# Kernel optimization log

Hardware: AMD Instinct MI355X
Metric: run time of the kernel (lower is better)

Reference implementation:

```python
import jax, jax.numpy as jnp
import numpy as np

BSZ = 2          # batch
H_IMG = 180      # BEV height
W_IMG = 180      # BEV width
BLK = 15         # block_size
D = 128          # d_model
NH = 8           # nhead
DH = D // NH     # head dim


def _bn_relu(x, g, b, m, v, eps=1e-5):
    # eval-mode BatchNorm2d followed by ReLU; x is NCHW
    s = g * jax.lax.rsqrt(v + eps)
    return jax.nn.relu((x - m[None, :, None, None]) * s[None, :, None, None]
                       + b[None, :, None, None])


def _split_tokens(x):
    # (B,C,H,W) -> (B*nb, blk*blk, C), block order = (row-block, col-block)
    B, C, H, W = x.shape
    hb, wb = H // BLK, W // BLK
    x = x.reshape(B, C, hb, BLK, wb, BLK)
    x = x.transpose(0, 2, 4, 1, 3, 5)              # (B,hb,wb,C,blk,blk)
    x = x.reshape(B * hb * wb, C, BLK * BLK)
    return x.transpose(0, 2, 1)                    # (B*nb, L, C)


def _merge_tokens(t, B, H, W):
    # (B*nb, L, C) -> (B,C,H,W), inverse of _split_tokens
    hb, wb = H // BLK, W // BLK
    C = t.shape[-1]
    x = t.transpose(0, 2, 1).reshape(B, hb, wb, C, BLK, BLK)
    x = x.transpose(0, 3, 1, 4, 2, 5)              # (B,C,hb,blk,wb,blk)
    return x.reshape(B, C, H, W)


def setup_inputs() -> dict:
    key = jax.random.key(0)
    ks = jax.random.split(key, 16)
    n = lambda i, shp, sc=0.05: jax.random.normal(ks[i], shp, jnp.float32) * sc
    inp = {
        'camera_feat': jax.random.normal(ks[0], (BSZ, 80, H_IMG, W_IMG), jnp.float32),
        'lidar_feat': jax.random.normal(ks[1], (BSZ, 256, H_IMG, W_IMG), jnp.float32),
        'cam_w': n(2, (D, 80)),
        'cam_gamma': jnp.ones((D,), jnp.float32),
        'cam_beta': jnp.zeros((D,), jnp.float32),
        'cam_mean': n(3, (D,)),
        'cam_var': jax.random.uniform(ks[4], (D,), jnp.float32, 0.5, 1.5),
        'lidar_w': n(5, (D, 256)),
        'lidar_gamma': jnp.ones((D,), jnp.float32),
        'lidar_beta': jnp.zeros((D,), jnp.float32),
        'lidar_mean': n(6, (D,)),
        'lidar_var': jax.random.uniform(ks[7], (D,), jnp.float32, 0.5, 1.5),
        'in_proj_w': n(8, (3 * D, D)),
        'in_proj_b': jnp.zeros((3 * D,), jnp.float32),
        'out_proj_w': n(9, (D, D)),
        'out_proj_b': jnp.zeros((D,), jnp.float32),
        'outc_w': n(10, (256, D, 3, 3)),
        'outc_gamma': jnp.ones((256,), jnp.float32),
        'outc_beta': jnp.zeros((256,), jnp.float32),
        'outc_mean': n(11, (256,)),
        'outc_var': jax.random.uniform(ks[12], (256,), jnp.float32, 0.5, 1.5),
    }
    return inp


def reference(camera_feat, lidar_feat,
              cam_w, cam_gamma, cam_beta, cam_mean, cam_var,
              lidar_w, lidar_gamma, lidar_beta, lidar_mean, lidar_var,
              in_proj_w, in_proj_b, out_proj_w, out_proj_b,
              outc_w, outc_gamma, outc_beta, outc_mean, outc_var):
    B, _, H, W = camera_feat.shape
    # 1x1 conv projections + BN + ReLU
    cam_p = _bn_relu(jnp.einsum('bchw,dc->bdhw', camera_feat, cam_w),
                     cam_gamma, cam_beta, cam_mean, cam_var)
    lid_p = _bn_relu(jnp.einsum('bchw,dc->bdhw', lidar_feat, lidar_w),
                     lidar_gamma, lidar_beta, lidar_mean, lidar_var)
    # windowed tokens: (B*nb, L=225, D)
    cam_t = _split_tokens(cam_p)
    lid_t = _split_tokens(lid_p)
    # cross-attention: query=lidar, key/value=camera (torch MHA math)
    wq, wk, wv = in_proj_w[:D], in_proj_w[D:2 * D], in_proj_w[2 * D:]
    bq, bk, bv = in_proj_b[:D], in_proj_b[D:2 * D], in_proj_b[2 * D:]
    BN, L, _ = lid_t.shape
    q = (lid_t @ wq.T + bq).reshape(BN, L, NH, DH).transpose(0, 2, 1, 3)
    k = (cam_t @ wk.T + bk).reshape(BN, L, NH, DH).transpose(0, 2, 1, 3)
    v = (cam_t @ wv.T + bv).reshape(BN, L, NH, DH).transpose(0, 2, 1, 3)
    scores = jnp.einsum('bhqd,bhkd->bhqk', q, k) / jnp.sqrt(jnp.float32(DH))
    attn = jax.nn.softmax(scores, axis=-1)
    ctx = jnp.einsum('bhqk,bhkd->bhqd', attn, v)
    ctx = ctx.transpose(0, 2, 1, 3).reshape(BN, L, D)
    attn_out = ctx @ out_proj_w.T + out_proj_b
    # merge windows back and fuse
    fused = _merge_tokens(attn_out, B, H, W) + lid_p
    # 3x3 conv + BN + ReLU
    y = jax.lax.conv_general_dilated(
        fused, outc_w, window_strides=(1, 1), padding='SAME',
        dimension_numbers=('NCHW', 'OIHW', 'NCHW'))
    return _bn_relu(y, outc_gamma, outc_beta, outc_mean, outc_var)
```

## Files before the change

kernel.cpp:

```cpp
#include <hip/hip_runtime.h>
#include <hip/hip_bf16.h>
#include <cmath>

#define HW      32400
#define WIMG    180
#define DD      128
#define NHEADS  8
#define DHEAD   16
#define LTOK    225
#define PSTRIDE 64928
#define FBROW   188
#define FBH     182
#define FBSZ    ((size_t)FBH * FBROW * 128)
#define QSCALE  0.36067376022224085f

typedef __attribute__((ext_vector_type(8))) short bf16x8;
typedef __attribute__((ext_vector_type(4))) float f32x4;

union U16B { uint4 u; int4 i; bf16x8 v; };

__device__ __forceinline__ bf16x8 ldfrag(const __hip_bfloat16* p, int ld, int lane) {
  return *(const bf16x8*)(p + (size_t)(lane & 15) * ld + ((lane >> 4) << 3));
}

__device__ __forceinline__ float bf2f(unsigned int u) {
  return __uint_as_float(u << 16);
}

__device__ __forceinline__ unsigned short f2bf(float x) {
  unsigned int b = __float_as_uint(x);
  return (unsigned short)((b + 0x7fffu + ((b >> 16) & 1u)) >> 16);
}

__global__ void k_cast(const float* __restrict__ in, __hip_bfloat16* __restrict__ out, int n) {
  int i = blockIdx.x * 256 + threadIdx.x;
  if (i < n) out[i] = __float2bfloat16(in[i]);
}

__global__ void k_prepproj(const float* __restrict__ w, __hip_bfloat16* __restrict__ wb,
                           int C, int Kpad) {
  int i = blockIdx.x * 256 + threadIdx.x;
  if (i >= 128 * Kpad) return;
  int d = i / Kpad, c = i % Kpad;
  wb[i] = (c < C) ? __float2bfloat16(w[d * C + c]) : __float2bfloat16(0.f);
}

__global__ void k_prepw2(const float* __restrict__ cw, __hip_bfloat16* __restrict__ wcb) {
  int i = blockIdx.x * 256 + threadIdx.x;
  if (i >= 294912) return;
  int oc16  = i / 18432;
  int r0    = i % 18432;
  int tap   = r0 / 2048;
  int r1    = r0 % 2048;
  int chunk = r1 / 512;
  int r2    = r1 % 512;
  int lane  = r2 / 8;
  int e     = r2 % 8;
  int oc = oc16 * 16 + (lane & 15);
  int ic = chunk * 32 + (lane >> 4) * 8 + e;
  wcb[i] = __float2bfloat16(cw[(size_t)(oc * 128 + ic) * 9 + tap]);
}

__global__ void k_zero_border(__hip_bfloat16* __restrict__ fbb) {
  int idx = blockIdx.x * 256 + threadIdx.x;
  if (idx >= 2 * 736 * 16) return;
  int b = idx / (736 * 16);
  int r = idx % (736 * 16);
  int px = r >> 4, blk = r & 15;
  int row, col;
  if (px < 188)      { row = 0;            col = px; }
  else if (px < 376) { row = 181;          col = px - 188; }
  else if (px < 556) { row = px - 376 + 1; col = 0; }
  else               { row = px - 556 + 1; col = 181; }
  ((uint4*)(fbb + (size_t)b * FBSZ + ((size_t)row * FBROW + col) * 128))[blk] =
      make_uint4(0u, 0u, 0u, 0u);
}

__global__ void __launch_bounds__(256) k_proj_mfma(
    const float* __restrict__ in, const __hip_bfloat16* __restrict__ wb,
    const float* __restrict__ g, const float* __restrict__ be,
    const float* __restrict__ mu, const float* __restrict__ var,
    __hip_bfloat16* __restrict__ outp, int C, int Kpad) {
  __shared__ __align__(16) __hip_bfloat16 sa[128 * 64];
  int m0 = blockIdx.x * 128;
  int b = blockIdx.z;
  int tid = threadIdx.x, lane = tid & 63, wid = tid >> 6;
  int wm = (wid >> 1) * 64, wn = (wid & 1) * 64;
  const float* inb = in + (size_t)b * C * HW;
  int sp = (tid >> 1) & 127;
  int sc4 = (tid & 1) * 4;
  int gp = m0 + sp;
  bool pok = gp < HW;
  f32x4 acc[4][4] = {};
  for (int kc = 0; kc < Kpad; kc += 64) {
    __syncthreads();
#pragma unroll
    for (int it = 0; it < 8; ++it) {
      int lc = sc4 + it * 8;
      int c = kc + lc;
      unsigned short u[4];
#pragma unroll
      for (int j = 0; j < 4; ++j) {
        float x = (pok && (c + j) < C) ? inb[(size_t)(c + j) * HW + gp] : 0.f;
        u[j] = f2bf(x);
      }
      int blk = (lc >> 3) ^ (sp & 7);
      char* dst = (char*)sa + sp * 128 + blk * 16 + (lc & 7) * 2;
      *(uint2*)dst = make_uint2(((unsigned)u[1] << 16) | u[0],
                                ((unsigned)u[3] << 16) | u[2]);
    }
    __syncthreads();
#pragma unroll
    for (int ks = 0; ks < 2; ++ks) {
      bf16x8 af[4], bfr[4];
#pragma unroll
      for (int i = 0; i < 4; ++i) {
        int pr = wm + i * 16 + (lane & 15);
        int blk = ((ks * 4 + (lane >> 4)) ^ (pr & 7));
        af[i] = *(const bf16x8*)((const char*)sa + pr * 128 + blk * 16);
      }
#pragma unroll
      for (int j = 0; j < 4; ++j)
        bfr[j] = ldfrag(wb + (size_t)(wn + j * 16) * Kpad + kc + ks * 32, Kpad, lane);
#pragma unroll
      for (int i = 0; i < 4; ++i)
#pragma unroll
        for (int j = 0; j < 4; ++j)
          acc[i][j] = __builtin_amdgcn_mfma_f32_16x16x32_bf16(af[i], bfr[j], acc[i][j], 0, 0, 0);
    }
  }
  int col = lane & 15, rq = lane >> 4;
  __hip_bfloat16* ob = outp + (size_t)b * PSTRIDE * 128;
#pragma unroll
  for (int j = 0; j < 4; ++j) {
    int d = wn + j * 16 + col;
    float s = g[d] * rsqrtf(var[d] + 1e-5f);
    float mm = mu[d], bb = be[d];
#pragma unroll
    for (int i = 0; i < 4; ++i) {
#pragma unroll
      for (int r = 0; r < 4; ++r) {
        int m = m0 + wm + i * 16 + rq * 4 + r;
        if (m < HW) {
          float y = (acc[i][j][r] - mm) * s + bb;
          ob[(size_t)m * 128 + d] = __float2bfloat16(fmaxf(y, 0.f));
        }
      }
    }
  }
}

__global__ void __launch_bounds__(256) k_gemm_bias(
    const __hip_bfloat16* __restrict__ A, const __hip_bfloat16* __restrict__ B,
    const float* __restrict__ bias, __hip_bfloat16* __restrict__ out,
    int K, int ldout, float oscale) {
  int m0 = blockIdx.x * 128, n0 = blockIdx.y * 128, b = blockIdx.z;
  int lane = threadIdx.x & 63, wid = threadIdx.x >> 6;
  int wm = (wid >> 1) * 64, wn = (wid & 1) * 64;
  const __hip_bfloat16* Ab = A + (size_t)b * PSTRIDE * K;
  f32x4 acc[4][4] = {};
  for (int kc = 0; kc < K; kc += 32) {
    bf16x8 af[4], bfr[4];
#pragma unroll
    for (int i = 0; i < 4; ++i)
      af[i] = ldfrag(Ab + (size_t)(m0 + wm + i * 16) * K + kc, K, lane);
#pragma unroll
    for (int j = 0; j < 4; ++j)
      bfr[j] = ldfrag(B + (size_t)(n0 + wn + j * 16) * K + kc, K, lane);
#pragma unroll
    for (int i = 0; i < 4; ++i)
#pragma unroll
      for (int j = 0; j < 4; ++j)
        acc[i][j] = __builtin_amdgcn_mfma_f32_16x16x32_bf16(af[i], bfr[j], acc[i][j], 0, 0, 0);
  }
  int col = lane & 15, rq = lane >> 4;
  __hip_bfloat16* ob = out + (size_t)b * PSTRIDE * ldout;
#pragma unroll
  for (int j = 0; j < 4; ++j) {
    int n = n0 + wn + j * 16 + col;
    float bs = bias[n];
#pragma unroll
    for (int i = 0; i < 4; ++i) {
#pragma unroll
      for (int r = 0; r < 4; ++r) {
        int m = m0 + wm + i * 16 + rq * 4 + r;
        if (m < HW) ob[(size_t)m * ldout + n] = __float2bfloat16((acc[i][j][r] + bs) * oscale);
      }
    }
  }
}

__global__ void __launch_bounds__(256) k_attn_mfma(
    const __hip_bfloat16* __restrict__ qc, const __hip_bfloat16* __restrict__ kvb,
    __hip_bfloat16* __restrict__ ctx) {
  __shared__ __align__(16) uint4 Kf[15 * 64];
  __shared__ __align__(16) uint4 Vf[15 * 64];
  __shared__ __align__(16) unsigned short psh[4 * 384];
  int bn = blockIdx.x, hh = blockIdx.y;
  int b = bn / 144, rr = bn % 144, tby = rr / 12, tbx = rr % 12;
  int tid = threadIdx.x;
  int pbase = tby * 15 * WIMG + tbx * 15;
  const __hip_bfloat16* kvbase = kvb + (size_t)b * PSTRIDE * 256 + hh * 16;

  if (tid < 240) {
    int row = tid;
    int ck = row >> 4, q = row & 15;
    uint4 k0 = make_uint4(0, 0, 0, 0), k1 = k0, v0 = k0, v1 = k0;
    if (row < LTOK) {
      int p = pbase + (row / 15) * WIMG + (row % 15);
      const uint4* kp = (const uint4*)(kvbase + (size_t)p * 256);
      k0 = kp[0]; k1 = kp[1];
      v0 = kp[16]; v1 = kp[17];
    }
    uint4 zz = make_uint4(0, 0, 0, 0);
    Kf[ck * 64 + q]      = k0;
    Kf[ck * 64 + 16 + q] = k1;
    Kf[ck * 64 + 32 + q] = zz;
    Kf[ck * 64 + 48 + q] = zz;
    unsigned short vv[16];
    *(uint4*)&vv[0] = v0;
    *(uint4*)&vv[8] = v1;
    int vg = q >> 3, vj = q & 7;
#pragma unroll
    for (int d0 = 0; d0 < 16; ++d0) {
      int d = (d0 + q + 2 * ck) & 15;
      ((unsigned short*)&Vf[ck * 64 + vg * 16 + d])[vj] = vv[d];
    }
    Vf[ck * 64 + 32 + q] = zz;
    Vf[ck * 64 + 48 + q] = zz;
  }
  __syncthreads();

  int lane = tid & 63, wid = tid >> 6;
  int g = lane >> 4, q15 = lane & 15;
  int wq0 = wid * 64;
  char* pw_base = (char*)psh + wid * 768;
  const bf16x8* KfB = (const bf16x8*)Kf + lane;
  const bf16x8* VfB = (const bf16x8*)Vf + lane;

  bf16x8 qf[4];
#pragma unroll
  for (int i = 0; i < 4; ++i) {
    int q = wq0 + i * 16 + q15;
    int qq = q < LTOK ? q : 0;
    int p = pbase + (qq / 15) * WIMG + (qq % 15);
    U16B u; u.u = make_uint4(0, 0, 0, 0);
    if (g < 2) u.u = *(const uint4*)(qc + ((size_t)b * PSTRIDE + p) * 128 + hh * 16 + g * 8);
    qf[i] = u.v;
  }

  const f32x4 zacc = {};
  float ls[4] = {0.f, 0.f, 0.f, 0.f};
  f32x4 oac[4] = {};
#pragma unroll 1
  for (int ck = 0; ck < 15; ++ck) {
    bf16x8 kf = KfB[ck * 64];
    bf16x8 vf = VfB[ck * 64];
#pragma unroll
    for (int i = 0; i < 4; ++i) {
      f32x4 st = __builtin_amdgcn_mfma_f32_16x16x32_bf16(kf, qf[i], zacc, 0, 0, 0);
      float p0 = exp2f(st[0]);
      float p1 = exp2f(st[1]);
      float p2 = exp2f(st[2]);
      float p3 = exp2f(st[3]);
      if (ck == 14) {
        if (g) p0 = 0.f;
        p1 = 0.f; p2 = 0.f; p3 = 0.f;
      }
      ls[i] += (p0 + p1) + (p2 + p3);
      unsigned w0 = (unsigned)__bfloat16_as_ushort(__float2bfloat16(p0)) |
                    ((unsigned)__bfloat16_as_ushort(__float2bfloat16(p1)) << 16);
      unsigned w1 = (unsigned)__bfloat16_as_ushort(__float2bfloat16(p2)) |
                    ((unsigned)__bfloat16_as_ushort(__float2bfloat16(p3)) << 16);
      *(uint2*)(pw_base + q15 * 48 + g * 8) = make_uint2(w0, w1);
      U16B pu;
      pu.u = *(const uint4*)(pw_base + q15 * 48 + (g & 1) * 16);
      oac[i] = __builtin_amdgcn_mfma_f32_16x16x32_bf16(vf, pu.v, oac[i], 0, 0, 0);
    }
  }
#pragma unroll
  for (int i = 0; i < 4; ++i) {
    ls[i] += __shfl_xor(ls[i], 16);
    ls[i] += __shfl_xor(ls[i], 32);
  }

  __hip_bfloat16* cb = ctx + (size_t)b * PSTRIDE * 128 + hh * 16;
#pragma unroll
  for (int i = 0; i < 4; ++i) {
    float inv = 1.f / ls[i];
    int qo = wq0 + i * 16 + q15;
    if (qo < LTOK) {
      unsigned lo = (unsigned)f2bf(oac[i][0] * inv) | ((unsigned)f2bf(oac[i][1] * inv) << 16);
      unsigned hi = (unsigned)f2bf(oac[i][2] * inv) | ((unsigned)f2bf(oac[i][3] * inv) << 16);
      int p = pbase + (qo / 15) * WIMG + (qo % 15);
      *(uint2*)(cb + (size_t)p * 128 + g * 4) = make_uint2(lo, hi);
    }
  }
}

__global__ void __launch_bounds__(256) k_outproj_mfma(
    const __hip_bfloat16* __restrict__ ctx, const __hip_bfloat16* __restrict__ wob,
    const float* __restrict__ opb, const __hip_bfloat16* __restrict__ lidb,
    __hip_bfloat16* __restrict__ fb) {
  int m0 = blockIdx.x * 128, b = blockIdx.z;
  int lane = threadIdx.x & 63, wid = threadIdx.x >> 6;
  int wm = (wid >> 1) * 64, wn = (wid & 1) * 64;
  const __hip_bfloat16* Ab = ctx + (size_t)b * PSTRIDE * 128;
  f32x4 acc[4][4] = {};
  for (int kc = 0; kc < 128; kc += 32) {
    bf16x8 af[4], bfr[4];
#pragma unroll
    for (int i = 0; i < 4; ++i)
      af[i] = ldfrag(Ab + (size_t)(m0 + wm + i * 16) * 128 + kc, 128, lane);
#pragma unroll
    for (int j = 0; j < 4; ++j)
      bfr[j] = ldfrag(wob + (size_t)(wn + j * 16) * 128 + kc, 128, lane);
#pragma unroll
    for (int i = 0; i < 4; ++i)
#pragma unroll
      for (int j = 0; j < 4; ++j)
        acc[i][j] = __builtin_amdgcn_mfma_f32_16x16x32_bf16(af[i], bfr[j], acc[i][j], 0, 0, 0);
  }
  int col = lane & 15, rq = lane >> 4;
  const __hip_bfloat16* lb = lidb + (size_t)b * PSTRIDE * 128;
  __hip_bfloat16* fbp = fb + (size_t)b * FBSZ;
#pragma unroll
  for (int j = 0; j < 4; ++j) {
    int n = wn + j * 16 + col;
    float bs = opb[n];
#pragma unroll
    for (int i = 0; i < 4; ++i) {
#pragma unroll
      for (int r = 0; r < 4; ++r) {
        int m = m0 + wm + i * 16 + rq * 4 + r;
        if (m < HW) {
          float v = acc[i][j][r] + bs + __bfloat162float(lb[(size_t)m * 128 + n]);
          int hhh = m / WIMG, www = m % WIMG;
          fbp[((size_t)(hhh + 1) * FBROW + (www + 1)) * 128 + n] = __float2bfloat16(v);
        }
      }
    }
  }
}

__global__ void __launch_bounds__(512) k_conv_mfma(
    const __hip_bfloat16* __restrict__ fb, const __hip_bfloat16* __restrict__ wcb,
    const float* __restrict__ g, const float* __restrict__ be,
    const float* __restrict__ mu, const float* __restrict__ var,
    float* __restrict__ out) {
  __shared__ __align__(16) uint4 Asm[4 * 16 * 62];
  int bx = blockIdx.x;
  int hp = bx / 3, strip = bx % 3;
  int h0 = hp * 2;
  int w0 = strip * 60;
  int b = blockIdx.z;
  int tid = threadIdx.x, lane = tid & 63, wid = tid >> 6;
  int q15 = lane & 15, kg = lane >> 4;
  int wpx = (wid & 1) * 32;
  int ocq = wid >> 1;
  const __hip_bfloat16* fbb = fb + (size_t)b * FBSZ;
  const __hip_bfloat16* Bw = wcb + (size_t)(ocq * 4) * 18432 + lane * 8;

#pragma unroll
  for (int it = 0; it < 8; ++it) {
    int slot = it * 512 + tid;
    if (slot < 3968) {
      int px = slot % 62;
      int rowk = slot / 62;
      int dy = rowk >> 4, kgrp = rowk & 15;
      Asm[slot] = *(const uint4*)(fbb + ((size_t)(h0 + dy) * FBROW + (w0 + px)) * 128 + kgrp * 8);
    }
  }

#define LOADB(dst, t)                                                          \
  {                                                                            \
    int tap_ = (t) >> 2, ch_ = (t) & 3;                                        \
    _Pragma("unroll") for (int j = 0; j < 4; ++j)                              \
        dst[j] = *(const bf16x8*)(Bw + (size_t)j * 18432 + tap_ * 2048 + ch_ * 512); \
  }

  bf16x8 bp0[4], bp1[4];
  LOADB(bp0, 0);
  LOADB(bp1, 1);
  __syncthreads();

  f32x4 acc[2][2][4] = {};

#define STEP(t, bp)                                                            \
  {                                                                            \
    int tap_ = (t) >> 2, ch_ = (t) & 3;                                        \
    int dy_ = tap_ / 3, dx_ = tap_ % 3;                                        \
    bf16x8 af[2][2];                                                           \
    _Pragma("unroll") for (int r = 0; r < 2; ++r) {                            \
      int rowk_ = ((dy_ + r) * 16 + ch_ * 4 + kg) * 62;                        \
      _Pragma("unroll") for (int i = 0; i < 2; ++i)                            \
          af[r][i] = *(const bf16x8*)&Asm[rowk_ + wpx + i * 16 + q15 + dx_];   \
    }                                                                          \
    _Pragma("unroll") for (int r = 0; r < 2; ++r)                              \
        _Pragma("unroll") for (int i = 0; i < 2; ++i)                          \
            _Pragma("unroll") for (int j = 0; j < 4; ++j)                      \
                acc[r][i][j] = __builtin_amdgcn_mfma_f32_16x16x32_bf16(af[r][i], bp[j], acc[r][i][j], 0, 0, 0); \
  }

#pragma unroll
  for (int t = 0; t < 36; t += 2) {
    STEP(t, bp0);
    if (t + 2 < 36) LOADB(bp0, t + 2);
    STEP(t + 1, bp1);
    if (t + 3 < 36) LOADB(bp1, t + 3);
  }
#undef STEP
#undef LOADB

  int ocbase = ocq * 64;
#pragma unroll
  for (int j = 0; j < 4; ++j) {
    int oc = ocbase + j * 16 + q15;
    float s = g[oc] * rsqrtf(var[oc] + 1e-5f);
    float mm = mu[oc], bb = be[oc];
#pragma unroll
    for (int r = 0; r < 2; ++r) {
#pragma unroll
      for (int i = 0; i < 2; ++i) {
        int pxb = wpx + i * 16 + kg * 4;
        if (pxb < 60) {
          float4 o4;
          o4.x = fmaxf((acc[r][i][j][0] - mm) * s + bb, 0.f);
          o4.y = fmaxf((acc[r][i][j][1] - mm) * s + bb, 0.f);
          o4.z = fmaxf((acc[r][i][j][2] - mm) * s + bb, 0.f);
          o4.w = fmaxf((acc[r][i][j][3] - mm) * s + bb, 0.f);
          *(float4*)(&out[(size_t)(b * 256 + oc) * HW + (h0 + r) * WIMG + w0 + pxb]) = o4;
        }
      }
    }
  }
}

extern "C" void kernel_launch(void* const* d_in, const int* in_sizes, int n_in,
                              void* d_out, int out_size, void* d_ws, size_t ws_size,
                              hipStream_t stream) {
  const float* camera = (const float*)d_in[0];
  const float* lidar  = (const float*)d_in[1];
  const float* cam_w  = (const float*)d_in[2];
  const float* cam_g  = (const float*)d_in[3];
  const float* cam_b  = (const float*)d_in[4];
  const float* cam_m  = (const float*)d_in[5];
  const float* cam_v  = (const float*)d_in[6];
  const float* lid_w  = (const float*)d_in[7];
  const float* lid_g  = (const float*)d_in[8];
  const float* lid_b  = (const float*)d_in[9];
  const float* lid_m  = (const float*)d_in[10];
  const float* lid_v  = (const float*)d_in[11];
  const float* ipw    = (const float*)d_in[12];
  const float* ipb    = (const float*)d_in[13];
  const float* opw    = (const float*)d_in[14];
  const float* opb    = (const float*)d_in[15];
  const float* ocw    = (const float*)d_in[16];
  const float* ocg    = (const float*)d_in[17];
  const float* ocb    = (const float*)d_in[18];
  const float* ocm    = (const float*)d_in[19];
  const float* ocv    = (const float*)d_in[20];

  __hip_bfloat16* ws = (__hip_bfloat16*)d_ws;
  const size_t NP = (size_t)2 * PSTRIDE * 128;
  __hip_bfloat16* cam_bf = ws;
  __hip_bfloat16* lid_bf = ws + NP;
  __hip_bfloat16* qc     = ws + 2 * NP;
  __hip_bfloat16* kvb    = ws + 3 * NP;
  __hip_bfloat16* wipb   = ws + 5 * NP;
  __hip_bfloat16* wob    = wipb + 384 * 128;
  __hip_bfloat16* wcb    = wob + 128 * 128;
  __hip_bfloat16* wcamb  = wcb + 256 * 9 * 128;
  __hip_bfloat16* wlidb  = wcamb + 128 * 128;
  __hip_bfloat16* fbbuf  = cam_bf;

  dim3 blk(256);
  hipLaunchKernelGGL(k_cast, dim3(192), blk, 0, stream, ipw, wipb, 384 * 128);
  hipLaunchKernelGGL(k_cast, dim3(64), blk, 0, stream, opw, wob, 128 * 128);
  hipLaunchKernelGGL(k_prepw2, dim3(1152), blk, 0, stream, ocw, wcb);
  hipLaunchKernelGGL(k_prepproj, dim3(64), blk, 0, stream, cam_w, wcamb, 80, 128);
  hipLaunchKernelGGL(k_prepproj, dim3(128), blk, 0, stream, lid_w, wlidb, 256, 256);
  dim3 gproj(254, 1, 2);
  hipLaunchKernelGGL(k_proj_mfma, gproj, blk, 0, stream,
                     camera, wcamb, cam_g, cam_b, cam_m, cam_v, cam_bf, 80, 128);
  hipLaunchKernelGGL(k_proj_mfma, gproj, blk, 0, stream,
                     lidar, wlidb, lid_g, lid_b, lid_m, lid_v, lid_bf, 256, 256);
  hipLaunchKernelGGL(k_gemm_bias, dim3(254, 1, 2), blk, 0, stream,
                     lid_bf, wipb, ipb, qc, 128, 128, QSCALE);
  hipLaunchKernelGGL(k_gemm_bias, dim3(254, 2, 2), blk, 0, stream,
                     cam_bf, wipb + 128 * 128, ipb + 128, kvb, 128, 256, 1.0f);
  hipLaunchKernelGGL(k_attn_mfma, dim3(288, 8), blk, 0, stream, qc, kvb, qc);
  hipLaunchKernelGGL(k_zero_border, dim3(92), blk, 0, stream, fbbuf);
  hipLaunchKernelGGL(k_outproj_mfma, dim3(254, 1, 2), blk, 0, stream,
                     qc, wob, opb, lid_bf, fbbuf);
  hipLaunchKernelGGL(k_conv_mfma, dim3(270, 1, 2), dim3(512), 0, stream,
                     fbbuf, wcb, ocg, ocb, ocm, ocv, (float*)d_out);
}
```

Baseline: 294.8 us.

## Merge weight prep kernels, use 16x16x16 MFMA in attention, halve conv LDS staging

Five weight-prep launches become one combined kernel, which removes launch overhead. The attention kernel switches to the 16x16x16 bf16 MFMA via inline asm. This drops the zero padding of K/V and the LDS round trip for P, since the probabilities are packed directly into registers. The conv kernel stages input channels in two halves to halve its LDS footprint, which may raise occupancy at the cost of an extra sync and a reload phase mid-loop.

```diff
diff --git a/kernel.cpp b/kernel.cpp
--- a/kernel.cpp
+++ b/kernel.cpp
@@ -15,9 +15,11 @@
 #define QSCALE  0.36067376022224085f
 
 typedef __attribute__((ext_vector_type(8))) short bf16x8;
+typedef __attribute__((ext_vector_type(4))) short bf16x4;
 typedef __attribute__((ext_vector_type(4))) float f32x4;
 
 union U16B { uint4 u; int4 i; bf16x8 v; };
+union U8B  { uint2 u; bf16x4 v; };
 
 __device__ __forceinline__ bf16x8 ldfrag(const __hip_bfloat16* p, int ld, int lane) {
   return *(const bf16x8*)(p + (size_t)(lane & 15) * ld + ((lane >> 4) << 3));
@@ -32,33 +34,40 @@
   return (unsigned short)((b + 0x7fffu + ((b >> 16) & 1u)) >> 16);
 }
 
-__global__ void k_cast(const float* __restrict__ in, __hip_bfloat16* __restrict__ out, int n) {
+__global__ void k_prep_all(
+    const float* __restrict__ ipw, const float* __restrict__ opw,
+    const float* __restrict__ ocw, const float* __restrict__ cam_w,
+    const float* __restrict__ lid_w,
+    __hip_bfloat16* __restrict__ wipb, __hip_bfloat16* __restrict__ wob,
+    __hip_bfloat16* __restrict__ wcb, __hip_bfloat16* __restrict__ wcamb,
+    __hip_bfloat16* __restrict__ wlidb) {
   int i = blockIdx.x * 256 + threadIdx.x;
-  if (i < n) out[i] = __float2bfloat16(in[i]);
-}
-
-__global__ void k_prepproj(const float* __restrict__ w, __hip_bfloat16* __restrict__ wb,
-                           int C, int Kpad) {
-  int i = blockIdx.x * 256 + threadIdx.x;
-  if (i >= 128 * Kpad) return;
-  int d = i / Kpad, c = i % Kpad;
-  wb[i] = (c < C) ? __float2bfloat16(w[d * C + c]) : __float2bfloat16(0.f);
-}
-
-__global__ void k_prepw2(const float* __restrict__ cw, __hip_bfloat16* __restrict__ wcb) {
-  int i = blockIdx.x * 256 + threadIdx.x;
-  if (i >= 294912) return;
-  int oc16  = i / 18432;
-  int r0    = i % 18432;
-  int tap   = r0 / 2048;
-  int r1    = r0 % 2048;
-  int chunk = r1 / 512;
-  int r2    = r1 % 512;
-  int lane  = r2 / 8;
-  int e     = r2 % 8;
-  int oc = oc16 * 16 + (lane & 15);
-  int ic = chunk * 32 + (lane >> 4) * 8 + e;
-  wcb[i] = __float2bfloat16(cw[(size_t)(oc * 128 + ic) * 9 + tap]);
+  if (i < 49152) { wipb[i] = __float2bfloat16(ipw[i]); return; }
+  i -= 49152;
+  if (i < 16384) { wob[i] = __float2bfloat16(opw[i]); return; }
+  i -= 16384;
+  if (i < 294912) {
+    int oc16  = i / 18432;
+    int r0    = i % 18432;
+    int tap   = r0 / 2048;
+    int r1    = r0 % 2048;
+    int chunk = r1 / 512;
+    int r2    = r1 % 512;
+    int lane  = r2 / 8;
+    int e     = r2 % 8;
+    int oc = oc16 * 16 + (lane & 15);
+    int ic = chunk * 32 + (lane >> 4) * 8 + e;
+    wcb[i] = __float2bfloat16(ocw[(size_t)(oc * 128 + ic) * 9 + tap]);
+    return;
+  }
+  i -= 294912;
+  if (i < 16384) {
+    int d = i / 128, c = i % 128;
+    wcamb[i] = (c < 80) ? __float2bfloat16(cam_w[d * 80 + c]) : __float2bfloat16(0.f);
+    return;
+  }
+  i -= 16384;
+  if (i < 32768) { wlidb[i] = __float2bfloat16(lid_w[i]); return; }
 }
 
 __global__ void k_zero_border(__hip_bfloat16* __restrict__ fbb) {
@@ -193,9 +202,8 @@
 __global__ void __launch_bounds__(256) k_attn_mfma(
     const __hip_bfloat16* __restrict__ qc, const __hip_bfloat16* __restrict__ kvb,
     __hip_bfloat16* __restrict__ ctx) {
-  __shared__ __align__(16) uint4 Kf[15 * 64];
-  __shared__ __align__(16) uint4 Vf[15 * 64];
-  __shared__ __align__(16) unsigned short psh[4 * 384];
+  __shared__ __align__(8) uint2 Kf[15 * 64];
+  __shared__ __align__(8) uint2 Vf[15 * 64];
   int bn = blockIdx.x, hh = blockIdx.y;
   int b = bn / 144, rr = bn % 144, tby = rr / 12, tbx = rr % 12;
   int tid = threadIdx.x;
@@ -212,53 +220,51 @@
       k0 = kp[0]; k1 = kp[1];
       v0 = kp[16]; v1 = kp[17];
     }
-    uint4 zz = make_uint4(0, 0, 0, 0);
-    Kf[ck * 64 + q]      = k0;
-    Kf[ck * 64 + 16 + q] = k1;
-    Kf[ck * 64 + 32 + q] = zz;
-    Kf[ck * 64 + 48 + q] = zz;
+    Kf[ck * 64 + q]      = make_uint2(k0.x, k0.y);
+    Kf[ck * 64 + 16 + q] = make_uint2(k0.z, k0.w);
+    Kf[ck * 64 + 32 + q] = make_uint2(k1.x, k1.y);
+    Kf[ck * 64 + 48 + q] = make_uint2(k1.z, k1.w);
     unsigned short vv[16];
     *(uint4*)&vv[0] = v0;
     *(uint4*)&vv[8] = v1;
-    int vg = q >> 3, vj = q & 7;
+    int vg = q >> 2, vj = q & 3;
+    unsigned short* vb = (unsigned short*)&Vf[ck * 64 + vg * 16];
 #pragma unroll
     for (int d0 = 0; d0 < 16; ++d0) {
-      int d = (d0 + q + 2 * ck) & 15;
-      ((unsigned short*)&Vf[ck * 64 + vg * 16 + d])[vj] = vv[d];
-    }
-    Vf[ck * 64 + 32 + q] = zz;
-    Vf[ck * 64 + 48 + q] = zz;
+      int d = (d0 + q) & 15;
+      vb[d * 4 + vj] = vv[d];
+    }
   }
   __syncthreads();
 
   int lane = tid & 63, wid = tid >> 6;
   int g = lane >> 4, q15 = lane & 15;
   int wq0 = wid * 64;
-  char* pw_base = (char*)psh + wid * 768;
-  const bf16x8* KfB = (const bf16x8*)Kf + lane;
-  const bf16x8* VfB = (const bf16x8*)Vf + lane;
-
-  bf16x8 qf[4];
+  const uint2* KfB = Kf + lane;
+  const uint2* VfB = Vf + lane;
+
+  bf16x4 qf[4];
 #pragma unroll
   for (int i = 0; i < 4; ++i) {
     int q = wq0 + i * 16 + q15;
     int qq = q < LTOK ? q : 0;
     int p = pbase + (qq / 15) * WIMG + (qq % 15);
-    U16B u; u.u = make_uint4(0, 0, 0, 0);
-    if (g < 2) u.u = *(const uint4*)(qc + ((size_t)b * PSTRIDE + p) * 128 + hh * 16 + g * 8);
+    U8B u;
+    u.u = *(const uint2*)(qc + ((size_t)b * PSTRIDE + p) * 128 + hh * 16 + g * 4);
     qf[i] = u.v;
   }
 
-  const f32x4 zacc = {};
   float ls[4] = {0.f, 0.f, 0.f, 0.f};
   f32x4 oac[4] = {};
 #pragma unroll 1
   for (int ck = 0; ck < 15; ++ck) {
-    bf16x8 kf = KfB[ck * 64];
-    bf16x8 vf = VfB[ck * 64];
+    U8B ku; ku.u = KfB[ck * 64];
+    U8B vu; vu.u = VfB[ck * 64];
+    bf16x4 kf = ku.v, vf = vu.v;
 #pragma unroll
     for (int i = 0; i < 4; ++i) {
-      f32x4 st = __builtin_amdgcn_mfma_f32_16x16x32_bf16(kf, qf[i], zacc, 0, 0, 0);
+      f32x4 st = {0.f, 0.f, 0.f, 0.f};
+      asm("v_mfma_f32_16x16x16_bf16 %0, %1, %2, %0" : "+v"(st) : "v"(kf), "v"(qf[i]));
       float p0 = exp2f(st[0]);
       float p1 = exp2f(st[1]);
       float p2 = exp2f(st[2]);
@@ -268,14 +274,10 @@
         p1 = 0.f; p2 = 0.f; p3 = 0.f;
       }
       ls[i] += (p0 + p1) + (p2 + p3);
-      unsigned w0 = (unsigned)__bfloat16_as_ushort(__float2bfloat16(p0)) |
-                    ((unsigned)__bfloat16_as_ushort(__float2bfloat16(p1)) << 16);
-      unsigned w1 = (unsigned)__bfloat16_as_ushort(__float2bfloat16(p2)) |
-                    ((unsigned)__bfloat16_as_ushort(__float2bfloat16(p3)) << 16);
-      *(uint2*)(pw_base + q15 * 48 + g * 8) = make_uint2(w0, w1);
-      U16B pu;
-      pu.u = *(const uint4*)(pw_base + q15 * 48 + (g & 1) * 16);
-      oac[i] = __builtin_amdgcn_mfma_f32_16x16x32_bf16(vf, pu.v, oac[i], 0, 0, 0);
+      U8B pu;
+      pu.u = make_uint2((unsigned)f2bf(p0) | ((unsigned)f2bf(p1) << 16),
+                        (unsigned)f2bf(p2) | ((unsigned)f2bf(p3) << 16));
+      asm("v_mfma_f32_16x16x16_bf16 %0, %1, %2, %0" : "+v"(oac[i]) : "v"(vf), "v"(pu.v));
     }
   }
 #pragma unroll
@@ -348,7 +350,7 @@
     const float* __restrict__ g, const float* __restrict__ be,
     const float* __restrict__ mu, const float* __restrict__ var,
     float* __restrict__ out) {
-  __shared__ __align__(16) uint4 Asm[4 * 16 * 62];
+  __shared__ __align__(16) uint4 Asm[4 * 8 * 62];
   int bx = blockIdx.x;
   int hp = bx / 3, strip = bx % 3;
   int h0 = hp * 2;
@@ -361,38 +363,34 @@
   const __hip_bfloat16* fbb = fb + (size_t)b * FBSZ;
   const __hip_bfloat16* Bw = wcb + (size_t)(ocq * 4) * 18432 + lane * 8;
 
-#pragma unroll
-  for (int it = 0; it < 8; ++it) {
-    int slot = it * 512 + tid;
-    if (slot < 3968) {
-      int px = slot % 62;
-      int rowk = slot / 62;
-      int dy = rowk >> 4, kgrp = rowk & 15;
-      Asm[slot] = *(const uint4*)(fbb + ((size_t)(h0 + dy) * FBROW + (w0 + px)) * 128 + kgrp * 8);
-    }
-  }
-
-#define LOADB(dst, t)                                                          \
+#define STAGEA(half)                                                           \
   {                                                                            \
-    int tap_ = (t) >> 2, ch_ = (t) & 3;                                        \
+    _Pragma("unroll") for (int it = 0; it < 4; ++it) {                         \
+      int slot = it * 512 + tid;                                               \
+      if (slot < 1984) {                                                       \
+        int px = slot % 62;                                                    \
+        int rowk = slot / 62;                                   \
+        int dy = rowk >> 3, k8 = rowk & 7;                                     \
+        Asm[slot] = *(const uint4*)(fbb + ((size_t)(h0 + dy) * FBROW + (w0 + px)) * 128 + ((half) * 8 + k8) * 8); \
+      }                                                                        \
+    }                                                                          \
+  }
+
+#define LOADB(dst, s)                                                          \
+  {                                                                            \
+    int half_ = (s) / 18, rem_ = (s) % 18, tap_ = rem_ / 2, ch2_ = rem_ & 1;   \
+    int chunk_ = half_ * 2 + ch2_;                                             \
     _Pragma("unroll") for (int j = 0; j < 4; ++j)                              \
-        dst[j] = *(const bf16x8*)(Bw + (size_t)j * 18432 + tap_ * 2048 + ch_ * 512); \
-  }
-
-  bf16x8 bp0[4], bp1[4];
-  LOADB(bp0, 0);
-  LOADB(bp1, 1);
-  __syncthreads();
-
-  f32x4 acc[2][2][4] = {};
-
-#define STEP(t, bp)                                                            \
+        dst[j] = *(const bf16x8*)(Bw + (size_t)j * 18432 + tap_ * 2048 + chunk_ * 512); \
+  }
+
+#define STEP(s, bp)                                                            \
   {                                                                            \
-    int tap_ = (t) >> 2, ch_ = (t) & 3;                                        \
+    int rem_ = (s) % 18, tap_ = rem_ / 2, ch2_ = rem_ & 1;                     \
     int dy_ = tap_ / 3, dx_ = tap_ % 3;                                        \
     bf16x8 af[2][2];                                                           \
     _Pragma("unroll") for (int r = 0; r < 2; ++r) {                            \
-      int rowk_ = ((dy_ + r) * 16 + ch_ * 4 + kg) * 62;                        \
+      int rowk_ = ((dy_ + r) * 8 + ch2_ * 4 + kg) * 62;                        \
       _Pragma("unroll") for (int i = 0; i < 2; ++i)                            \
           af[r][i] = *(const bf16x8*)&Asm[rowk_ + wpx + i * 16 + q15 + dx_];   \
     }                                                                          \
@@ -402,15 +400,34 @@
                 acc[r][i][j] = __builtin_amdgcn_mfma_f32_16x16x32_bf16(af[r][i], bp[j], acc[r][i][j], 0, 0, 0); \
   }
 
-#pragma unroll
-  for (int t = 0; t < 36; t += 2) {
-    STEP(t, bp0);
-    if (t + 2 < 36) LOADB(bp0, t + 2);
-    STEP(t + 1, bp1);
-    if (t + 3 < 36) LOADB(bp1, t + 3);
+  bf16x8 bp0[4], bp1[4];
+  STAGEA(0);
+  LOADB(bp0, 0);
+  LOADB(bp1, 1);
+  __syncthreads();
+
+  f32x4 acc[2][2][4] = {};
+
+#pragma unroll
+  for (int s = 0; s < 18; s += 2) {
+    STEP(s, bp0);
+    LOADB(bp0, s + 2);
+    STEP(s + 1, bp1);
+    LOADB(bp1, s + 3);
+  }
+  __syncthreads();
+  STAGEA(1);
+  __syncthreads();
+#pragma unroll
+  for (int s = 18; s < 36; s += 2) {
+    STEP(s, bp0);
+    if (s + 2 < 36) LOADB(bp0, s + 2);
+    STEP(s + 1, bp1);
+    if (s + 3 < 36) LOADB(bp1, s + 3);
   }
 #undef STEP
 #undef LOADB
+#undef STAGEA
 
   int ocbase = ocq * 64;
 #pragma unroll
@@ -475,11 +492,8 @@
   __hip_bfloat16* fbbuf  = cam_bf;
 
   dim3 blk(256);
-  hipLaunchKernelGGL(k_cast, dim3(192), blk, 0, stream, ipw, wipb, 384 * 128);
-  hipLaunchKernelGGL(k_cast, dim3(64), blk, 0, stream, opw, wob, 128 * 128);
-  hipLaunchKernelGGL(k_prepw2, dim3(1152), blk, 0, stream, ocw, wcb);
-  hipLaunchKernelGGL(k_prepproj, dim3(64), blk, 0, stream, cam_w, wcamb, 80, 128);
-  hipLaunchKernelGGL(k_prepproj, dim3(128), blk, 0, stream, lid_w, wlidb, 256, 256);
+  hipLaunchKernelGGL(k_prep_all, dim3(1600), blk, 0, stream,
+                     ipw, opw, ocw, cam_w, lid_w, wipb, wob, wcb, wcamb, wlidb);
   dim3 gproj(254, 1, 2);
   hipLaunchKernelGGL(k_proj_mfma, gproj, blk, 0, stream,
                      camera, wcamb, cam_g, cam_b, cam_m, cam_v, cam_bf, 80, 128);
```

Measured after the change: 292.0 us. No clear change (-0.9%).
